# Kernel tuning notes

Hardware: AMD Instinct MI355X
Metric: run time of the kernel (lower is better)

The kernel has to match this reference:

```python
import jax, jax.numpy as jnp
import numpy as np

OUT_RANGE = 6.0
OUT_SHIFT = -3.0


def setup_inputs() -> dict:
    key = jax.random.key(0)
    ks = jax.random.split(key, 6)
    B, T = 128, 64
    A, V, X = 48, 48, 96
    PF = 128
    fdim = (A + 1) * (V + 1) * (X + 1)  # 232897
    return {
        "audio_h": jax.random.normal(ks[0], (B, T, A), jnp.float32),
        "video_h": jax.random.normal(ks[1], (B, T, V), jnp.float32),
        "text_h": jax.random.normal(ks[2], (B, T, X), jnp.float32),
        "W1": jax.random.normal(ks[3], (fdim, PF), jnp.float32) * 0.002,
        "b1": jnp.zeros((PF,), jnp.float32),
        "W2": jax.random.normal(ks[4], (PF, PF), jnp.float32) * 0.05,
        "b2": jnp.zeros((PF,), jnp.float32),
        "W3": jax.random.normal(ks[5], (PF, 1), jnp.float32) * 0.05,
        "b3": jnp.zeros((1,), jnp.float32),
    }


def reference(audio_h, video_h, text_h, W1, b1, W2, b2, W3, b3):
    B, T, A = audio_h.shape
    V = video_h.shape[-1]
    X = text_h.shape[-1]
    one = jnp.ones((B, T, 1), audio_h.dtype)
    a = jnp.concatenate([one, audio_h], axis=-1)  # [B,T,A+1]
    v = jnp.concatenate([one, video_h], axis=-1)  # [B,T,V+1]
    x = jnp.concatenate([one, text_h], axis=-1)   # [B,T,X+1]
    # per-timestep triple outer product, summed over t.
    # flatten order matches torch: audio slowest, then video, text fastest.
    av = jnp.einsum("bta,btv->btav", a, v).reshape(B, T, (A + 1) * (V + 1))
    fusion = jnp.einsum("btp,btx->bpx", av, x).reshape(B, -1)  # [B,(A+1)(V+1)(X+1)]
    # dropout is identity in eval mode
    h1 = jax.nn.relu(fusion @ W1 + b1)
    h2 = jax.nn.relu(h1 @ W2 + b2)
    out = jax.nn.sigmoid(h2 @ W3 + b3) * OUT_RANGE + OUT_SHIFT  # [B,1] in (-3,3)
    return out
```

## Files before the change

kernel.cpp:

```cpp
#include <hip/hip_runtime.h>


#define B_    128
#define T_    64
#define A1    49
#define V1    49
#define X1    97
#define IJ    2401
#define KTOT  232897
#define FP    232928
#define PF    128
#define KC    256
#define NB2   910

typedef short s8v __attribute__((ext_vector_type(8)));
typedef float f4v __attribute__((ext_vector_type(4)));

__device__ __forceinline__ unsigned short f2bf(float f) {
    union { float f; unsigned u; } v; v.f = f;
    return (unsigned short)((v.u + 0x7FFFu + ((v.u >> 16) & 1u)) >> 16);
}

__global__ __launch_bounds__(512) void k1_fusion(
    const float* __restrict__ audio, const float* __restrict__ video,
    const float* __restrict__ text, unsigned short* __restrict__ fusion)
{
    __shared__ float a_s[T_ * A1];
    __shared__ float v_s[T_ * V1];
    __shared__ unsigned short xT[112 * 72];
    __shared__ unsigned short w_ws[8][16 * 72];

    const int b = blockIdx.y;
    const int bx = blockIdx.x;
    const int tid = threadIdx.x;

    for (int idx = tid; idx < T_ * A1; idx += 512) {
        int t = idx / 49, i = idx - t * 49;
        a_s[idx] = (i == 0) ? 1.0f : audio[(b * T_ + t) * 48 + (i - 1)];
        v_s[idx] = (i == 0) ? 1.0f : video[(b * T_ + t) * 48 + (i - 1)];
    }
    for (int idx = tid; idx < T_ * X1; idx += 512) {
        int t = idx / 97, k = idx - t * 97;
        xT[k * 72 + t] = f2bf((k == 0) ? 1.0f : text[(b * T_ + t) * 96 + (k - 1)]);
    }
    for (int idx = tid; idx < 15 * 64; idx += 512) {
        xT[(97 + (idx >> 6)) * 72 + (idx & 63)] = 0;
    }
    __syncthreads();

    const int wave = tid >> 6, lane = tid & 63;
    const int q = lane >> 4, ln = lane & 15;
    unsigned short* w_s = w_ws[wave];

    for (int it = 0; it < 5; ++it) {
        const int tw = it * 8 + wave;
        if (tw >= 38) break;
        const int tl = bx * 38 + tw;
        if (tl >= 151) break;
        const int ij0 = tl * 16;

        #pragma unroll
        for (int ijl = 0; ijl < 16; ++ijl) {
            int ij = ij0 + ijl;
            unsigned short wv = 0;
            if (ij < IJ) {
                int i = ij / 49, j = ij - i * 49;
                wv = f2bf(a_s[lane * 49 + i] * v_s[lane * 49 + j]);
            }
            w_s[ijl * 72 + lane] = wv;
        }
        s8v af0 = *(const s8v*)&w_s[ln * 72 + q * 8];
        s8v af1 = *(const s8v*)&w_s[ln * 72 + 32 + q * 8];
        #pragma unroll
        for (int nt = 0; nt < 7; ++nt) {
            s8v bf0 = *(const s8v*)&xT[(nt * 16 + ln) * 72 + q * 8];
            s8v bf1 = *(const s8v*)&xT[(nt * 16 + ln) * 72 + 32 + q * 8];
            f4v acc = {0.f, 0.f, 0.f, 0.f};
            acc = __builtin_amdgcn_mfma_f32_16x16x32_bf16(af0, bf0, acc, 0, 0, 0);
            acc = __builtin_amdgcn_mfma_f32_16x16x32_bf16(af1, bf1, acc, 0, 0, 0);
            int kk = nt * 16 + ln;
            if (kk < X1) {
                #pragma unroll
                for (int r = 0; r < 4; ++r) {
                    int ij = ij0 + q * 4 + r;
                    if (ij < IJ)
                        fusion[(size_t)b * FP + ij * X1 + kk] = f2bf(acc[r]);
                }
            }
        }
    }
}

template<bool TAIL>
__device__ __forceinline__ void k2_body(
    const unsigned short* __restrict__ fusion, const float* __restrict__ W1,
    float* __restrict__ partials, int blk)
{
    const int kbase = blk * KC;
    const int tid = threadIdx.x;
    const int wave = tid >> 6, lane = tid & 63;
    const int q = lane >> 4, ln = lane & 15;
    const int f = wave * 16 + ln;

    f4v acc[8];
    #pragma unroll
    for (int m = 0; m < 8; ++m) acc[m] = (f4v){0.f, 0.f, 0.f, 0.f};

    #pragma unroll 2
    for (int s = 0; s < 8; ++s) {
        const int p0 = kbase + s * 32;
        s8v bfrag;
        #pragma unroll
        for (int j = 0; j < 8; ++j) {
            int p = p0 + q * 8 + j;
            float w;
            if (TAIL)
                w = (p < KTOT) ? W1[(size_t)p * PF + f] : 0.f;
            else
                w = __builtin_nontemporal_load(&W1[(size_t)p * PF + f]);
            ((unsigned short*)&bfrag)[j] = f2bf(w);
        }
        #pragma unroll
        for (int m = 0; m < 8; ++m) {
            s8v afrag = *(const s8v*)&fusion[(size_t)(m * 16 + ln) * FP + p0 + q * 8];
            acc[m] = __builtin_amdgcn_mfma_f32_16x16x32_bf16(afrag, bfrag, acc[m], 0, 0, 0);
        }
    }

    float* outp = partials + (size_t)blk * 16384;
    #pragma unroll
    for (int m = 0; m < 8; ++m) {
        #pragma unroll
        for (int r = 0; r < 4; ++r)
            outp[(m * 16 + q * 4 + r) * 128 + f] = acc[m][r];
    }
}

__global__ __launch_bounds__(512) void k2_gemm(
    const unsigned short* __restrict__ fusion, const float* __restrict__ W1,
    float* __restrict__ partials)
{
    const int blk = blockIdx.x;
    if (blk == NB2 - 1) k2_body<true>(fusion, W1, partials, blk);
    else                k2_body<false>(fusion, W1, partials, blk);
}

__global__ __launch_bounds__(256) void k3_reduce(
    const float* __restrict__ partials, const float* __restrict__ b1,
    float* __restrict__ h1)
{
    __shared__ float red[256];
    const int e = blockIdx.x * 32 + (threadIdx.x & 31);
    const int rh = threadIdx.x >> 5;
    float s0 = 0.f, s1 = 0.f;
    int r = rh;
    for (; r + 8 < NB2; r += 16) {
        s0 += partials[(size_t)r * 16384 + e];
        s1 += partials[(size_t)(r + 8) * 16384 + e];
    }
    for (; r < NB2; r += 8) s0 += partials[(size_t)r * 16384 + e];
    red[threadIdx.x] = s0 + s1;
    __syncthreads();
    if (threadIdx.x < 32) {
        float v = 0.f;
        #pragma unroll
        for (int g = 0; g < 8; ++g) v += red[g * 32 + threadIdx.x];
        v += b1[e & 127];
        h1[e] = fmaxf(v, 0.f);
    }
}

__global__ __launch_bounds__(128) void k45_tail(
    const float* __restrict__ h1, const float* __restrict__ W2,
    const float* __restrict__ b2, const float* __restrict__ W3,
    const float* __restrict__ b3, float* __restrict__ out)
{
    __shared__ float hrow[128];
    __shared__ float h2s[128];
    const int b = blockIdx.x, f = threadIdx.x;
    hrow[f] = h1[b * 128 + f];
    __syncthreads();
    float s = b2[f];
    #pragma unroll 8
    for (int c = 0; c < 128; ++c) s += hrow[c] * W2[c * 128 + f];
    h2s[f] = fmaxf(s, 0.f) * W3[f];
    __syncthreads();
    if (f < 64) {
        float v = h2s[f] + h2s[f + 64];
        #pragma unroll
        for (int off = 32; off > 0; off >>= 1)
            v += __shfl_down(v, off, 64);
        if (f == 0) out[b] = 6.0f / (1.0f + expf(-(v + b3[0]))) - 3.0f;
    }
}

extern "C" void kernel_launch(void* const* d_in, const int* in_sizes, int n_in,
                              void* d_out, int out_size, void* d_ws, size_t ws_size,
                              hipStream_t stream)
{
    const float* audio = (const float*)d_in[0];
    const float* video = (const float*)d_in[1];
    const float* text  = (const float*)d_in[2];
    const float* W1 = (const float*)d_in[3];
    const float* b1 = (const float*)d_in[4];
    const float* W2 = (const float*)d_in[5];
    const float* b2 = (const float*)d_in[6];
    const float* W3 = (const float*)d_in[7];
    const float* b3 = (const float*)d_in[8];
    float* out = (float*)d_out;

    char* ws = (char*)d_ws;
    unsigned short* fusion = (unsigned short*)ws;
    float* partials = (float*)(ws + 59629568);
    float* h1 = (float*)(ws + 119267328);

    k1_fusion<<<dim3(4, 128), 512, 0, stream>>>(audio, video, text, fusion);
    k2_gemm<<<dim3(NB2), 512, 0, stream>>>(fusion, W1, partials);
    k3_reduce<<<dim3(512), 256, 0, stream>>>(partials, b1, h1);
    k45_tail<<<dim3(128), 128, 0, stream>>>(h1, W2, b2, W3, b3, out);
}
```

Baseline: 303.8 us.

## Software-pipeline GEMM loads, halve split-K blocks, build fusion A-fragments in registers

k2 now handles 512-wide K chunks (455 blocks instead of 910) and double-buffers the W1 and fusion fragment loads in registers so the next step's global loads are issued before the current step's MFMAs. The tail block uses 15 steps with a guarded final load. This halves the partial-sum buffer and the k3 reduction traffic but raises register pressure, and the larger chunks may leave fewer blocks per CU. k1 now builds the A-fragments directly in registers from transposed audio/video tiles instead of staging them through shared memory, using 256-thread blocks on an 8x128 grid.

```diff
diff --git a/kernel.cpp b/kernel.cpp
--- a/kernel.cpp
+++ b/kernel.cpp
@@ -10,8 +10,9 @@
 #define KTOT  232897
 #define FP    232928
 #define PF    128
-#define KC    256
-#define NB2   910
+#define KC    512
+#define NB2   455
+#define NTILES 151
 
 typedef short s8v __attribute__((ext_vector_type(8)));
 typedef float f4v __attribute__((ext_vector_type(4)));
@@ -21,56 +22,57 @@
     return (unsigned short)((v.u + 0x7FFFu + ((v.u >> 16) & 1u)) >> 16);
 }
 
-__global__ __launch_bounds__(512) void k1_fusion(
+__global__ __launch_bounds__(256) void k1_fusion(
     const float* __restrict__ audio, const float* __restrict__ video,
     const float* __restrict__ text, unsigned short* __restrict__ fusion)
 {
-    __shared__ float a_s[T_ * A1];
-    __shared__ float v_s[T_ * V1];
+    __shared__ float aT[49 * 68];
+    __shared__ float vT[49 * 68];
     __shared__ unsigned short xT[112 * 72];
-    __shared__ unsigned short w_ws[8][16 * 72];
 
     const int b = blockIdx.y;
     const int bx = blockIdx.x;
     const int tid = threadIdx.x;
 
-    for (int idx = tid; idx < T_ * A1; idx += 512) {
-        int t = idx / 49, i = idx - t * 49;
-        a_s[idx] = (i == 0) ? 1.0f : audio[(b * T_ + t) * 48 + (i - 1)];
-        v_s[idx] = (i == 0) ? 1.0f : video[(b * T_ + t) * 48 + (i - 1)];
-    }
-    for (int idx = tid; idx < T_ * X1; idx += 512) {
+    for (int idx = tid; idx < 49 * 64; idx += 256) {
+        int i = idx >> 6, t = idx & 63;
+        aT[i * 68 + t] = (i == 0) ? 1.0f : audio[(b * 64 + t) * 48 + (i - 1)];
+        vT[i * 68 + t] = (i == 0) ? 1.0f : video[(b * 64 + t) * 48 + (i - 1)];
+    }
+    for (int idx = tid; idx < 64 * 97; idx += 256) {
         int t = idx / 97, k = idx - t * 97;
-        xT[k * 72 + t] = f2bf((k == 0) ? 1.0f : text[(b * T_ + t) * 96 + (k - 1)]);
-    }
-    for (int idx = tid; idx < 15 * 64; idx += 512) {
+        xT[k * 72 + t] = f2bf((k == 0) ? 1.0f : text[(b * 64 + t) * 96 + (k - 1)]);
+    }
+    for (int idx = tid; idx < 15 * 64; idx += 256)
         xT[(97 + (idx >> 6)) * 72 + (idx & 63)] = 0;
-    }
     __syncthreads();
 
     const int wave = tid >> 6, lane = tid & 63;
     const int q = lane >> 4, ln = lane & 15;
-    unsigned short* w_s = w_ws[wave];
-
+
+    #pragma unroll
     for (int it = 0; it < 5; ++it) {
-        const int tw = it * 8 + wave;
-        if (tw >= 38) break;
-        const int tl = bx * 38 + tw;
-        if (tl >= 151) break;
+        const int tw = it * 4 + wave;
+        const int tl = bx * 19 + tw;
+        if (tw >= 19 || tl >= NTILES) continue;
         const int ij0 = tl * 16;
 
-        #pragma unroll
-        for (int ijl = 0; ijl < 16; ++ijl) {
-            int ij = ij0 + ijl;
-            unsigned short wv = 0;
-            if (ij < IJ) {
-                int i = ij / 49, j = ij - i * 49;
-                wv = f2bf(a_s[lane * 49 + i] * v_s[lane * 49 + j]);
-            }
-            w_s[ijl * 72 + lane] = wv;
+        const int ij = ij0 + ln;
+        const bool valid = ij < IJ;
+        const int ijc = valid ? ij : IJ - 1;
+        const int i = ijc / 49, j2 = ijc - i * 49;
+        const float* ar = &aT[i * 68 + q * 8];
+        const float* vr = &vT[j2 * 68 + q * 8];
+
+        s8v af0, af1;
+        #pragma unroll
+        for (int j = 0; j < 8; ++j) {
+            float w0 = ar[j] * vr[j];
+            float w1 = ar[32 + j] * vr[32 + j];
+            ((unsigned short*)&af0)[j] = valid ? f2bf(w0) : (unsigned short)0;
+            ((unsigned short*)&af1)[j] = valid ? f2bf(w1) : (unsigned short)0;
         }
-        s8v af0 = *(const s8v*)&w_s[ln * 72 + q * 8];
-        s8v af1 = *(const s8v*)&w_s[ln * 72 + 32 + q * 8];
+
         #pragma unroll
         for (int nt = 0; nt < 7; ++nt) {
             s8v bf0 = *(const s8v*)&xT[(nt * 16 + ln) * 72 + q * 8];
@@ -82,16 +84,16 @@
             if (kk < X1) {
                 #pragma unroll
                 for (int r = 0; r < 4; ++r) {
-                    int ij = ij0 + q * 4 + r;
-                    if (ij < IJ)
-                        fusion[(size_t)b * FP + ij * X1 + kk] = f2bf(acc[r]);
+                    int ijr = ij0 + q * 4 + r;
+                    if (ijr < IJ)
+                        fusion[(size_t)b * FP + ijr * X1 + kk] = f2bf(acc[r]);
                 }
             }
         }
     }
 }
 
-template<bool TAIL>
+template<int NSTEPS, bool GUARD>
 __device__ __forceinline__ void k2_body(
     const unsigned short* __restrict__ fusion, const float* __restrict__ W1,
     float* __restrict__ partials, int blk)
@@ -106,43 +108,63 @@
     #pragma unroll
     for (int m = 0; m < 8; ++m) acc[m] = (f4v){0.f, 0.f, 0.f, 0.f};
 
-    #pragma unroll 2
-    for (int s = 0; s < 8; ++s) {
-        const int p0 = kbase + s * 32;
-        s8v bfrag;
-        #pragma unroll
-        for (int j = 0; j < 8; ++j) {
-            int p = p0 + q * 8 + j;
-            float w;
-            if (TAIL)
-                w = (p < KTOT) ? W1[(size_t)p * PF + f] : 0.f;
-            else
-                w = __builtin_nontemporal_load(&W1[(size_t)p * PF + f]);
-            ((unsigned short*)&bfrag)[j] = f2bf(w);
+    s8v a_cur[8], a_nxt[8];
+    float bw_cur[8], bw_nxt[8];
+
+    #pragma unroll
+    for (int j = 0; j < 8; ++j)
+        bw_cur[j] = __builtin_nontemporal_load(
+            &W1[(size_t)(kbase + q * 8 + j) * PF + f]);
+    #pragma unroll
+    for (int m = 0; m < 8; ++m)
+        a_cur[m] = *(const s8v*)&fusion[(size_t)(m * 16 + ln) * FP + kbase + q * 8];
+
+    #pragma unroll
+    for (int s = 0; s < NSTEPS; ++s) {
+        if (s + 1 < NSTEPS) {
+            const int p0 = kbase + (s + 1) * 32 + q * 8;
+            if (GUARD && (s + 1 == NSTEPS - 1)) {
+                #pragma unroll
+                for (int j = 0; j < 8; ++j)
+                    bw_nxt[j] = (p0 + j < KTOT) ? W1[(size_t)(p0 + j) * PF + f] : 0.f;
+            } else {
+                #pragma unroll
+                for (int j = 0; j < 8; ++j)
+                    bw_nxt[j] = __builtin_nontemporal_load(&W1[(size_t)(p0 + j) * PF + f]);
+            }
+            #pragma unroll
+            for (int m = 0; m < 8; ++m)
+                a_nxt[m] = *(const s8v*)&fusion[(size_t)(m * 16 + ln) * FP +
+                                                kbase + (s + 1) * 32 + q * 8];
         }
-        #pragma unroll
-        for (int m = 0; m < 8; ++m) {
-            s8v afrag = *(const s8v*)&fusion[(size_t)(m * 16 + ln) * FP + p0 + q * 8];
-            acc[m] = __builtin_amdgcn_mfma_f32_16x16x32_bf16(afrag, bfrag, acc[m], 0, 0, 0);
-        }
+        s8v bf;
+        #pragma unroll
+        for (int j = 0; j < 8; ++j)
+            ((unsigned short*)&bf)[j] = f2bf(bw_cur[j]);
+        #pragma unroll
+        for (int m = 0; m < 8; ++m)
+            acc[m] = __builtin_amdgcn_mfma_f32_16x16x32_bf16(a_cur[m], bf, acc[m], 0, 0, 0);
+        #pragma unroll
+        for (int m = 0; m < 8; ++m) a_cur[m] = a_nxt[m];
+        #pragma unroll
+        for (int j = 0; j < 8; ++j) bw_cur[j] = bw_nxt[j];
     }
 
     float* outp = partials + (size_t)blk * 16384;
     #pragma unroll
-    for (int m = 0; m < 8; ++m) {
+    for (int m = 0; m < 8; ++m)
         #pragma unroll
         for (int r = 0; r < 4; ++r)
             outp[(m * 16 + q * 4 + r) * 128 + f] = acc[m][r];
-    }
-}
-
-__global__ __launch_bounds__(512) void k2_gemm(
+}
+
+__global__ __launch_bounds__(512, 4) void k2_gemm(
     const unsigned short* __restrict__ fusion, const float* __restrict__ W1,
     float* __restrict__ partials)
 {
     const int blk = blockIdx.x;
-    if (blk == NB2 - 1) k2_body<true>(fusion, W1, partials, blk);
-    else                k2_body<false>(fusion, W1, partials, blk);
+    if (blk == NB2 - 1) k2_body<15, true>(fusion, W1, partials, blk);
+    else                k2_body<16, false>(fusion, W1, partials, blk);
 }
 
 __global__ __launch_bounds__(256) void k3_reduce(
@@ -212,9 +234,9 @@
     char* ws = (char*)d_ws;
     unsigned short* fusion = (unsigned short*)ws;
     float* partials = (float*)(ws + 59629568);
-    float* h1 = (float*)(ws + 119267328);
-
-    k1_fusion<<<dim3(4, 128), 512, 0, stream>>>(audio, video, text, fusion);
+    float* h1 = (float*)(ws + 89448448);
+
+    k1_fusion<<<dim3(8, 128), 256, 0, stream>>>(audio, video, text, fusion);
     k2_gemm<<<dim3(NB2), 512, 0, stream>>>(fusion, W1, partials);
     k3_reduce<<<dim3(512), 256, 0, stream>>>(partials, b1, h1);
     k45_tail<<<dim3(128), 128, 0, stream>>>(h1, W2, b2, W3, b3, out);
```

After: 313.2 us. 1.03x slower.
